# Optimization experiments

Measured on AMD Instinct MI355X. Metric: run time of the kernel, lower is better.

The kernel has to match this reference:

```python
import jax, jax.numpy as jnp
import numpy as np

C, D, B, NS = 1000, 256, 16384, 200000
MOMENTUM = 0.1
TOPK = 5
EPS = 1e-12  # torch F.normalize default eps


def _cos_distance(a, b):
    # 0.5 * (1 - cos_sim) between rows of a [N,D] and rows of b [M,D]
    a = a / jnp.maximum(jnp.linalg.norm(a, axis=1, keepdims=True), EPS)
    b = b / jnp.maximum(jnp.linalg.norm(b, axis=1, keepdims=True), EPS)
    return 0.5 * (1.0 - jnp.einsum('nd,md->nm', a, b))


def setup_inputs() -> dict:
    key = jax.random.key(0)
    k1, k2, k3, k4 = jax.random.split(key, 4)
    return {
        'feature_source': jax.random.normal(k1, (B, D), jnp.float32),
        'center_mem': jax.random.normal(k2, (C, D), jnp.float32),
        'source_mem': jax.random.normal(k3, (NS, D), jnp.float32),
        'class2center': jnp.zeros((C, 2), jnp.float32),
        'interdist': jnp.zeros((C, C, 2), jnp.float32),
        'label_source': jax.random.randint(k4, (B,), 0, C, jnp.int32),
        'index_source': jnp.arange(B, dtype=jnp.int32),
    }


def reference(feature_source, center_mem, source_mem, class2center, interdist,
              label_source, index_source):
    # --- featuredistance2center: scatter-add per-class count and distance ---
    d1 = _cos_distance(feature_source, center_mem)            # [B, C]
    dist_at_label = jnp.take_along_axis(d1, label_source[:, None], axis=1)[:, 0]  # [B]
    class2center_new = class2center.at[label_source, 0].add(1.0)
    class2center_new = class2center_new.at[label_source, 1].add(dist_at_label)

    # --- update_center (labels_value=None): center += sum of features per class ---
    center_new = center_mem + jax.ops.segment_sum(feature_source, label_source,
                                                  num_segments=C)  # [C, D]

    # --- update_source: momentum scatter update of the source feature bank ---
    old = source_mem[index_source]                             # [B, D]
    source_mem_new = source_mem.at[index_source].set((1.0 - MOMENTUM) * old
                                                     + MOMENTUM * feature_source)

    # --- sourcefeature2differertcenter: topk-smallest distances, scatter-add ---
    d2 = _cos_distance(feature_source, center_new)             # [B, C]
    neg_vals, top_idx = jax.lax.top_k(-d2, TOPK)               # smallest distances
    top_dists = -neg_vals                                      # [B, TOPK]
    top1, top2 = top_idx[:, 0], top_idx[:, 1]
    inter = jnp.abs(top_dists[:, 0] - top_dists[:, 1])         # [B]
    interdist_new = interdist.at[top1, top2, 0].add(1.0)
    interdist_new = interdist_new.at[top1, top2, 1].add(inter)

    return (center_new, source_mem_new, class2center_new, interdist_new)
```

## Files before the change

kernel.cpp:

```cpp
#include <hip/hip_runtime.h>
#include <math.h>

#define Cc 1000
#define Cpad 1024
#define Dd 256
#define Bb 16384
#define NSs 200000
#define MOM 0.1f
#define EPSV 1e-12f
#define EPSC 0.10f
#define NEG_BIG (-3.4e38f)
#define IDX_BIG 0x7fffffff

#define OUT_CENTER 0
#define OUT_SRC (Cc*Dd)
#define OUT_C2C (OUT_SRC + (size_t)NSs*Dd)
#define OUT_INTER (OUT_C2C + Cc*2)

#define SCR_SCORES 0
#define SCR_FB 8388608
#define SCR_CB (SCR_FB + 2097152)

#define WS_CHAT 0
#define WS_INVF 256000
#define WS_MARK 272384

typedef __bf16    bf16x8 __attribute__((ext_vector_type(8)));
typedef float     f32x4  __attribute__((ext_vector_type(4)));
typedef _Float16  f16x8  __attribute__((ext_vector_type(8)));

__device__ __forceinline__ ushort f2bf(float f) {
    uint u = __float_as_uint(f);
    u += 0x7FFFu + ((u >> 16) & 1u);
    return (ushort)(u >> 16);
}

__device__ __forceinline__ void gload16(const void* g, void* l) {
    __builtin_amdgcn_global_load_lds(
        (const __attribute__((address_space(1))) void*)g,
        (__attribute__((address_space(3))) void*)l, 16, 0, 0);
}

__device__ __forceinline__ void upd_top2(float& s1, int& i1, float& s2, int& i2,
                                         float s, int i) {
    if (s > s1 || (s == s1 && i < i1)) {
        s2 = s1; i2 = i1; s1 = s; i1 = i;
    } else if (s > s2 || (s == s2 && i < i2)) {
        s2 = s; i2 = i;
    }
}

#define N_INTER4 (Cc*Cc*2/4)
#define N_C2C4   (Cc*2/4)
#define N_CM4    (Cc*Dd/4)
#define N_MARK4  (NSs/4)
#define N_INIT4  (N_INTER4 + N_C2C4 + N_CM4 + N_MARK4)

__global__ void k_init(const float4* __restrict__ interdist,
                       const float4* __restrict__ c2c,
                       const float4* __restrict__ cmem,
                       float4* __restrict__ out_inter,
                       float4* __restrict__ out_c2c,
                       float4* __restrict__ out_center,
                       int4* __restrict__ mark) {
    int i = blockIdx.x * blockDim.x + threadIdx.x;
    if (i < N_INTER4) {
        out_inter[i] = interdist[i];
    } else if (i < N_INTER4 + N_C2C4) {
        out_c2c[i - N_INTER4] = c2c[i - N_INTER4];
    } else if (i < N_INTER4 + N_C2C4 + N_CM4) {
        out_center[i - N_INTER4 - N_C2C4] = cmem[i - N_INTER4 - N_C2C4];
    } else if (i < N_INIT4) {
        int4 m; m.x = -1; m.y = -1; m.z = -1; m.w = -1;
        mark[i - N_INTER4 - N_C2C4 - N_CM4] = m;
    }
}

__global__ void k_rows_a(const float* __restrict__ feat, const float* __restrict__ cmem,
                         const int* __restrict__ label, const int* __restrict__ index,
                         float* __restrict__ out_center, float* __restrict__ out_c2c,
                         float* __restrict__ ws_invf, ushort* __restrict__ fb,
                         int* __restrict__ mark) {
    int wid  = threadIdx.x >> 6;
    int lane = threadIdx.x & 63;
    int row  = blockIdx.x * 4 + wid;
    if (row >= Bb) return;

    const float4 f4 = *(const float4*)(feat + (size_t)row * Dd + lane * 4);
    int lab = label[row];
    const float4 c4 = *(const float4*)(cmem + (size_t)lab * Dd + lane * 4);

    ushort4 h;
    h.x = f2bf(f4.x); h.y = f2bf(f4.y); h.z = f2bf(f4.z); h.w = f2bf(f4.w);
    *(ushort4*)(fb + (size_t)row * Dd + lane * 4) = h;

    float fs = f4.x*f4.x + f4.y*f4.y + f4.z*f4.z + f4.w*f4.w;
    float dt = f4.x*c4.x + f4.y*c4.y + f4.z*c4.z + f4.w*c4.w;
    float cs = c4.x*c4.x + c4.y*c4.y + c4.z*c4.z + c4.w*c4.w;
    #pragma unroll
    for (int off = 32; off; off >>= 1) {
        fs += __shfl_xor(fs, off);
        dt += __shfl_xor(dt, off);
        cs += __shfl_xor(cs, off);
    }
    float invf = 1.0f / fmaxf(sqrtf(fs), EPSV);
    if (lane == 0) {
        ws_invf[row] = invf;
        mark[index[row]] = row;
        float invc = 1.0f / fmaxf(sqrtf(cs), EPSV);
        float d1 = 0.5f * (1.0f - dt * invf * invc);
        atomicAdd(out_c2c + lab * 2,     1.0f);
        atomicAdd(out_c2c + lab * 2 + 1, d1);
    }
    atomicAdd(out_center + (size_t)lab * Dd + lane * 4 + 0, f4.x);
    atomicAdd(out_center + (size_t)lab * Dd + lane * 4 + 1, f4.y);
    atomicAdd(out_center + (size_t)lab * Dd + lane * 4 + 2, f4.z);
    atomicAdd(out_center + (size_t)lab * Dd + lane * 4 + 3, f4.w);
}

__global__ void k_chat(const float* __restrict__ out_center, float* __restrict__ chat,
                       ushort* __restrict__ cb) {
    int c = blockIdx.x;
    int lane = threadIdx.x;
    if (c >= Cc) {
        ushort4 z; z.x = 0; z.y = 0; z.z = 0; z.w = 0;
        *(ushort4*)(cb + (size_t)c * Dd + lane * 4) = z;
        return;
    }
    float4 v = *(const float4*)(out_center + (size_t)c * Dd + lane * 4);
    float ss = v.x*v.x + v.y*v.y + v.z*v.z + v.w*v.w;
    #pragma unroll
    for (int off = 32; off; off >>= 1) ss += __shfl_xor(ss, off);
    float inv = 1.0f / fmaxf(sqrtf(ss), EPSV);
    float4 r; r.x = v.x*inv; r.y = v.y*inv; r.z = v.z*inv; r.w = v.w*inv;
    *(float4*)(chat + (size_t)c * Dd + lane * 4) = r;
    ushort4 h;
    h.x = f2bf(r.x); h.y = f2bf(r.y); h.z = f2bf(r.z); h.w = f2bf(r.w);
    *(ushort4*)(cb + (size_t)c * Dd + lane * 4) = h;
}

__global__ __launch_bounds__(256, 3) void k_gemm(const ushort* __restrict__ fb,
                                                 const ushort* __restrict__ cb,
                                                 _Float16* __restrict__ scores) {
    __shared__ __align__(16) char Asb[128 * 128];
    __shared__ __align__(16) char Bsb[128 * 128];

    int tid  = threadIdx.x;
    int wid  = tid >> 6;
    int lane = tid & 63;
    int rl = lane & 15;
    int kg = lane >> 4;
    int wr = wid >> 1;
    int wc = wid & 1;
    int row0 = blockIdx.y * 128;
    int c0   = blockIdx.x * 128;

    int realb = ((lane & 7) ^ (lane >> 3)) << 4;

    f32x4 acc[4][4];
    f32x4 z = {0.f, 0.f, 0.f, 0.f};
    #pragma unroll
    for (int mi = 0; mi < 4; mi++)
        #pragma unroll
        for (int ni = 0; ni < 4; ni++)
            acc[mi][ni] = z;

    for (int t = 0; t < 4; t++) {
        #pragma unroll
        for (int i = 0; i < 4; i++) {
            int rloc = wid * 32 + i * 8;
            int grow = row0 + rloc + (lane >> 3);
            gload16((const char*)(fb + (size_t)grow * Dd) + t * 128 + realb,
                    Asb + rloc * 128);
        }
        #pragma unroll
        for (int i = 0; i < 4; i++) {
            int rloc = wid * 32 + i * 8;
            int gcol = c0 + rloc + (lane >> 3);
            gload16((const char*)(cb + (size_t)gcol * Dd) + t * 128 + realb,
                    Bsb + rloc * 128);
        }
        asm volatile("s_waitcnt vmcnt(0)" ::: "memory");
        __syncthreads();

        bf16x8 a[4][2], b[4][2];
        #pragma unroll
        for (int mi = 0; mi < 4; mi++)
            #pragma unroll
            for (int ks = 0; ks < 2; ks++) {
                int r = wr * 64 + mi * 16 + rl;
                int off = r * 128 + ((ks * 64 + kg * 16) ^ ((r & 7) << 4));
                a[mi][ks] = *(const bf16x8*)(Asb + off);
            }
        #pragma unroll
        for (int ni = 0; ni < 4; ni++)
            #pragma unroll
            for (int ks = 0; ks < 2; ks++) {
                int r = wc * 64 + ni * 16 + rl;
                int off = r * 128 + ((ks * 64 + kg * 16) ^ ((r & 7) << 4));
                b[ni][ks] = *(const bf16x8*)(Bsb + off);
            }

        #pragma unroll
        for (int ks = 0; ks < 2; ks++)
            #pragma unroll
            for (int mi = 0; mi < 4; mi++)
                #pragma unroll
                for (int ni = 0; ni < 4; ni++)
                    acc[mi][ni] = __builtin_amdgcn_mfma_f32_16x16x32_bf16(
                        a[mi][ks], b[ni][ks], acc[mi][ni], 0, 0, 0);

        __syncthreads();
    }

    #pragma unroll
    for (int mi = 0; mi < 4; mi++) {
        int row = row0 + wr * 64 + mi * 16 + kg * 4;
        #pragma unroll
        for (int ni = 0; ni < 4; ni++) {
            int col = c0 + wc * 64 + ni * 16 + rl;
            #pragma unroll
            for (int rr = 0; rr < 4; rr++)
                scores[(size_t)(row + rr) * Cpad + col] = (_Float16)acc[mi][ni][rr];
        }
    }
}

__global__ __launch_bounds__(256) void k_sel(const _Float16* __restrict__ scores,
                                             const float* __restrict__ feat,
                                             const float* __restrict__ chat,
                                             const float* __restrict__ ws_invf,
                                             float* __restrict__ out_inter) {
    __shared__ int cnt[4];
    __shared__ int clist[4][32];
    int wid  = threadIdx.x >> 6;
    int lane = threadIdx.x & 63;
    int row  = blockIdx.x * 4 + wid;
    if (lane == 0) cnt[wid] = 0;

    const f16x8* sp = (const f16x8*)(scores + (size_t)row * Cpad);
    float v[16];
    float s1 = NEG_BIG, s2 = NEG_BIG;
    int   i1 = IDX_BIG, i2 = IDX_BIG;
    #pragma unroll
    for (int k = 0; k < 2; k++) {
        f16x8 q = sp[k * 64 + lane];
        int cbase = k * 512 + lane * 8;
        #pragma unroll
        for (int e = 0; e < 8; e++) {
            float f = (float)q[e];
            v[k*8 + e] = f;
            int c = cbase + e;
            if (c < Cc) upd_top2(s1, i1, s2, i2, f, c);
        }
    }
    #pragma unroll
    for (int off = 1; off < 64; off <<= 1) {
        float ps1 = __shfl_xor(s1, off), ps2 = __shfl_xor(s2, off);
        int   pi1 = __shfl_xor(i1, off), pi2 = __shfl_xor(i2, off);
        upd_top2(s1, i1, s2, i2, ps1, pi1);
        upd_top2(s1, i1, s2, i2, ps2, pi2);
    }
    float thr = s2 - EPSC;
    #pragma unroll
    for (int j = 0; j < 16; j++) {
        int c = (j >> 3) * 512 + lane * 8 + (j & 7);
        if (v[j] >= thr && c < Cc) {
            int slot = atomicAdd(&cnt[wid], 1);
            if (slot < 32) clist[wid][slot] = c;
        }
    }
    __syncthreads();
    int n = cnt[wid]; if (n > 32) n = 32;

    const float4 f4 = *(const float4*)(feat + (size_t)row * Dd + lane * 4);
    float S1 = NEG_BIG, S2 = NEG_BIG;
    int   I1 = IDX_BIG, I2 = IDX_BIG;
    for (int k = 0; k < n; k++) {
        int c = clist[wid][k];
        const float4 c4 = *(const float4*)(chat + (size_t)c * Dd + lane * 4);
        float d = f4.x*c4.x + f4.y*c4.y + f4.z*c4.z + f4.w*c4.w;
        #pragma unroll
        for (int off = 32; off; off >>= 1) d += __shfl_xor(d, off);
        upd_top2(S1, I1, S2, I2, d, c);
    }
    if (lane == 0) {
        float inter = 0.5f * ws_invf[row] * (S1 - S2);
        size_t off2 = ((size_t)I1 * Cc + I2) * 2;
        atomicAdd(out_inter + off2,     1.0f);
        atomicAdd(out_inter + off2 + 1, inter);
    }
}

__global__ void k_src(const float* __restrict__ src, const float* __restrict__ feat,
                      const int* __restrict__ mark, float* __restrict__ dst) {
    const int n4 = NSs * Dd / 4;
    int stride = gridDim.x * blockDim.x;
    for (int e = blockIdx.x * blockDim.x + threadIdx.x; e < n4; e += stride) {
        int row = e >> 6;
        int m = mark[row];
        f32x4 v = __builtin_nontemporal_load((const f32x4*)src + e);
        if (m >= 0) {
            f32x4 f = *((const f32x4*)feat + (size_t)m * 64 + (e & 63));
            v = (1.0f - MOM) * v + MOM * f;
        }
        __builtin_nontemporal_store(v, (f32x4*)dst + e);
    }
}

extern "C" void kernel_launch(void* const* d_in, const int* in_sizes, int n_in,
                              void* d_out, int out_size, void* d_ws, size_t ws_size,
                              hipStream_t stream) {
    const float* feat   = (const float*)d_in[0];
    const float* cmem   = (const float*)d_in[1];
    const float* smem   = (const float*)d_in[2];
    const float* c2c    = (const float*)d_in[3];
    const float* inter  = (const float*)d_in[4];
    const int*   label  = (const int*)d_in[5];
    const int*   index  = (const int*)d_in[6];

    float* out = (float*)d_out;
    float* out_center = out + OUT_CENTER;
    float* out_src    = out + OUT_SRC;
    float* out_c2c    = out + OUT_C2C;
    float* out_inter  = out + OUT_INTER;

    float* ws    = (float*)d_ws;
    float* chat  = ws + WS_CHAT;
    float* winvf = ws + WS_INVF;
    int*   mark  = (int*)(ws + WS_MARK);

    _Float16* scores = (_Float16*)(out_src + SCR_SCORES);
    ushort*   fb     = (ushort*)(out_src + SCR_FB);
    ushort*   cb     = (ushort*)(out_src + SCR_CB);

    k_init<<<(N_INIT4 + 255) / 256, 256, 0, stream>>>(
        (const float4*)inter, (const float4*)c2c, (const float4*)cmem,
        (float4*)out_inter, (float4*)out_c2c, (float4*)out_center,
        (int4*)mark);
    k_rows_a<<<Bb / 4, 256, 0, stream>>>(feat, cmem, label, index,
                                         out_center, out_c2c, winvf, fb, mark);
    k_chat<<<Cpad, 64, 0, stream>>>(out_center, chat, cb);
    {
        dim3 grid(Cpad / 128, Bb / 128);
        k_gemm<<<grid, 256, 0, stream>>>(fb, cb, scores);
    }
    k_sel<<<Bb / 4, 256, 0, stream>>>(scores, feat, chat, winvf, out_inter);
    k_src<<<4096, 256, 0, stream>>>(smem, feat, mark, out_src);
}
```

Measured before the change: 261.4 us.

## Overlap source-bank copy with GEMM by co-scheduling copy blocks in one launch

Merges the bf16 GEMM and most of the source-memory momentum copy into a single launch. Within each group of four blocks, one does a GEMM tile and three stream part of the 200k-row bank, so the memory-bound copy can overlap the compute-bound GEMM. Rows that alias the scratch area in out_src (scores, fb, cb, up to SAFE_ROW) are left for a separate k_src2 launch after k_sel, so scratch data is not overwritten before it is read. The risk is that copy blocks compete with GEMM blocks for occupancy and bandwidth, and the launch_bounds(256,3) LDS footprint also applies to the copy blocks.

```diff
diff --git a/kernel.cpp b/kernel.cpp
--- a/kernel.cpp
+++ b/kernel.cpp
@@ -20,6 +20,10 @@
 #define SCR_SCORES 0
 #define SCR_FB 8388608
 #define SCR_CB (SCR_FB + 2097152)
+#define SCR_END 10616832
+#define SAFE_ROW 41472
+#define E0 (SAFE_ROW * 64)
+#define N4ALL (NSs * 64)
 
 #define WS_CHAT 0
 #define WS_INVF 256000
@@ -47,6 +51,23 @@
         s2 = s1; i2 = i1; s1 = s; i1 = i;
     } else if (s > s2 || (s == s2 && i < i2)) {
         s2 = s; i2 = i;
+    }
+}
+
+__device__ __forceinline__ void copy_range(const float* __restrict__ src,
+                                           const float* __restrict__ feat,
+                                           const int* __restrict__ mark,
+                                           float* __restrict__ dst,
+                                           int e0, int e1, int tid0, int nthreads) {
+    for (int e = e0 + tid0; e < e1; e += nthreads) {
+        int row = e >> 6;
+        int m = mark[row];
+        f32x4 v = __builtin_nontemporal_load((const f32x4*)src + e);
+        if (m >= 0) {
+            f32x4 f = *((const f32x4*)feat + (size_t)m * 64 + (e & 63));
+            v = (1.0f - MOM) * v + MOM * f;
+        }
+        __builtin_nontemporal_store(v, (f32x4*)dst + e);
     }
 }
 
@@ -139,11 +160,30 @@
     *(ushort4*)(cb + (size_t)c * Dd + lane * 4) = h;
 }
 
-__global__ __launch_bounds__(256, 3) void k_gemm(const ushort* __restrict__ fb,
-                                                 const ushort* __restrict__ cb,
-                                                 _Float16* __restrict__ scores) {
+#define GEMM_BLKS 1024
+#define COPY_BLKS 3072
+#define TOTAL_BLKS 4096
+
+__global__ __launch_bounds__(256, 3) void k_gemm_copy(const ushort* __restrict__ fb,
+                                                      const ushort* __restrict__ cb,
+                                                      _Float16* __restrict__ scores,
+                                                      const float* __restrict__ smem,
+                                                      const float* __restrict__ feat,
+                                                      const int* __restrict__ mark,
+                                                      float* __restrict__ out_src) {
     __shared__ __align__(16) char Asb[128 * 128];
     __shared__ __align__(16) char Bsb[128 * 128];
+
+    int b = blockIdx.x;
+    if ((b & 3) != 0) {
+        int c = (b - (b >> 2)) - 1;
+        int tid0 = c * 256 + threadIdx.x;
+        copy_range(smem, feat, mark, out_src, E0, N4ALL, tid0, COPY_BLKS * 256);
+        return;
+    }
+    int g = b >> 2;
+    int bx = g & 7;
+    int by = g >> 3;
 
     int tid  = threadIdx.x;
     int wid  = tid >> 6;
@@ -152,8 +192,8 @@
     int kg = lane >> 4;
     int wr = wid >> 1;
     int wc = wid & 1;
-    int row0 = blockIdx.y * 128;
-    int c0   = blockIdx.x * 128;
+    int row0 = by * 128;
+    int c0   = bx * 128;
 
     int realb = ((lane & 7) ^ (lane >> 3)) << 4;
 
@@ -183,7 +223,7 @@
         asm volatile("s_waitcnt vmcnt(0)" ::: "memory");
         __syncthreads();
 
-        bf16x8 a[4][2], b[4][2];
+        bf16x8 a[4][2], bfr[4][2];
         #pragma unroll
         for (int mi = 0; mi < 4; mi++)
             #pragma unroll
@@ -198,7 +238,7 @@
             for (int ks = 0; ks < 2; ks++) {
                 int r = wc * 64 + ni * 16 + rl;
                 int off = r * 128 + ((ks * 64 + kg * 16) ^ ((r & 7) << 4));
-                b[ni][ks] = *(const bf16x8*)(Bsb + off);
+                bfr[ni][ks] = *(const bf16x8*)(Bsb + off);
             }
 
         #pragma unroll
@@ -208,7 +248,7 @@
                 #pragma unroll
                 for (int ni = 0; ni < 4; ni++)
                     acc[mi][ni] = __builtin_amdgcn_mfma_f32_16x16x32_bf16(
-                        a[mi][ks], b[ni][ks], acc[mi][ni], 0, 0, 0);
+                        a[mi][ks], bfr[ni][ks], acc[mi][ni], 0, 0, 0);
 
         __syncthreads();
     }
@@ -292,20 +332,10 @@
     }
 }
 
-__global__ void k_src(const float* __restrict__ src, const float* __restrict__ feat,
-                      const int* __restrict__ mark, float* __restrict__ dst) {
-    const int n4 = NSs * Dd / 4;
-    int stride = gridDim.x * blockDim.x;
-    for (int e = blockIdx.x * blockDim.x + threadIdx.x; e < n4; e += stride) {
-        int row = e >> 6;
-        int m = mark[row];
-        f32x4 v = __builtin_nontemporal_load((const f32x4*)src + e);
-        if (m >= 0) {
-            f32x4 f = *((const f32x4*)feat + (size_t)m * 64 + (e & 63));
-            v = (1.0f - MOM) * v + MOM * f;
-        }
-        __builtin_nontemporal_store(v, (f32x4*)dst + e);
-    }
+__global__ void k_src2(const float* __restrict__ src, const float* __restrict__ feat,
+                       const int* __restrict__ mark, float* __restrict__ dst) {
+    int tid0 = blockIdx.x * blockDim.x + threadIdx.x;
+    copy_range(src, feat, mark, dst, 0, E0, tid0, gridDim.x * blockDim.x);
 }
 
 extern "C" void kernel_launch(void* const* d_in, const int* in_sizes, int n_in,
@@ -341,10 +371,8 @@
     k_rows_a<<<Bb / 4, 256, 0, stream>>>(feat, cmem, label, index,
                                          out_center, out_c2c, winvf, fb, mark);
     k_chat<<<Cpad, 64, 0, stream>>>(out_center, chat, cb);
-    {
-        dim3 grid(Cpad / 128, Bb / 128);
-        k_gemm<<<grid, 256, 0, stream>>>(fb, cb, scores);
-    }
+    k_gemm_copy<<<TOTAL_BLKS, 256, 0, stream>>>(fb, cb, scores,
+                                                smem, feat, mark, out_src);
     k_sel<<<Bb / 4, 256, 0, stream>>>(scores, feat, chat, winvf, out_inter);
-    k_src<<<4096, 256, 0, stream>>>(smem, feat, mark, out_src);
-}
+    k_src2<<<2048, 256, 0, stream>>>(smem, feat, mark, out_src);
+}
```

New measurement: 253.1 us, median of 2. -3.1%, faster.
